# Kernel tuning notes

Measured on AMD Instinct MI355X. Metric: run time of the kernel, lower is better.

Reference implementation:

```python
import jax, jax.numpy as jnp
import numpy as np

NUM_HEADS = 4
GROUPS = 8          # min(8, ch) with ch=256
EPS = 1e-5          # torch GroupNorm default eps


def setup_inputs() -> dict:
    key = jax.random.key(0)
    ks = jax.random.split(key, 3)
    b, c, h, w = 8, 256, 32, 32
    x = jax.random.normal(ks[0], (b, c, h, w), jnp.float32)
    gn_gamma = jnp.ones((c,), jnp.float32)
    gn_beta = jnp.zeros((c,), jnp.float32)
    qkv_w = jax.random.normal(ks[1], (3 * c, c), jnp.float32) * (c ** -0.5)
    qkv_b = jnp.zeros((3 * c,), jnp.float32)
    proj_w = jax.random.normal(ks[2], (c, c), jnp.float32) * (c ** -0.5)
    proj_b = jnp.zeros((c,), jnp.float32)
    return {"x": x, "gn_gamma": gn_gamma, "gn_beta": gn_beta,
            "qkv_w": qkv_w, "qkv_b": qkv_b, "proj_w": proj_w, "proj_b": proj_b}


def _group_norm(x, gamma, beta):
    b, c, h, w = x.shape
    xg = x.reshape(b, GROUPS, c // GROUPS, h, w)
    mean = xg.mean(axis=(2, 3, 4), keepdims=True)
    var = xg.var(axis=(2, 3, 4), keepdims=True)
    xn = ((xg - mean) * jax.lax.rsqrt(var + EPS)).reshape(b, c, h, w)
    return xn * gamma[None, :, None, None] + beta[None, :, None, None]


def reference(x, gn_gamma, gn_beta, qkv_w, qkv_b, proj_w, proj_b):
    b, c, h, w = x.shape
    dh = c // NUM_HEADS
    xn = _group_norm(x, gn_gamma, gn_beta)
    # 1x1 conv == channel matmul
    qkv = jnp.einsum('oc,bchw->bohw', qkv_w, xn) + qkv_b[None, :, None, None]
    qkv = qkv.reshape(b, 3, NUM_HEADS, dh, h * w)
    q, k, v = qkv[:, 0], qkv[:, 1], qkv[:, 2]   # each (b, n, dh, hw)
    scale = dh ** -0.5
    # full (hw x hw) attention matrix, matching the original explicit einsum
    attn = jax.nn.softmax(jnp.einsum('bncd,bnce->bnde', q, k) * scale, axis=-1)
    out = jnp.einsum('bnde,bnce->bncd', attn, v).reshape(b, c, h, w)
    out = jnp.einsum('oc,bchw->bohw', proj_w, out) + proj_b[None, :, None, None]
    return x + out
```

## Files before the change

kernel.cpp:

```cpp
#include <hip/hip_runtime.h>
#include <stdint.h>

typedef __attribute__((ext_vector_type(8))) short short8;
typedef __attribute__((ext_vector_type(4))) float f32x4;

#define BB 8
#define CC 256
#define PP 1024
#define NH 4
#define DH 64

#define QSCALE 0.18033688f

__device__ __forceinline__ unsigned short f2bf(float f) {
  union { float f; unsigned u; } v; v.f = f;
  unsigned r = v.u + 0x7FFFu + ((v.u >> 16) & 1u);
  return (unsigned short)(r >> 16);
}

__device__ __forceinline__ f32x4 mfma16(short8 a, short8 b, f32x4 c) {
  return __builtin_amdgcn_mfma_f32_16x16x32_bf16(a, b, c, 0, 0, 0);
}

__global__ __launch_bounds__(256) void prep(
    const float* __restrict__ x, float2* __restrict__ part,
    const float* __restrict__ qkvw, const float* __restrict__ projw,
    unsigned short* __restrict__ wall) {
  int blk = blockIdx.x;
  int tid = threadIdx.x;
  if (blk < 512) {
    int sl = blk & 7, g = (blk >> 3) & 7, b = blk >> 6;
    const float4* xb =
        (const float4*)(x + (size_t)(b * CC + g * 32) * PP) + sl * 1024;
    float s = 0.f, q = 0.f;
    for (int i = tid; i < 1024; i += 256) {
      float4 v = xb[i];
      s += v.x + v.y + v.z + v.w;
      q += v.x * v.x + v.y * v.y + v.z * v.z + v.w * v.w;
    }
    for (int off = 32; off > 0; off >>= 1) {
      s += __shfl_down(s, off);
      q += __shfl_down(q, off);
    }
    __shared__ float rs[4], rq[4];
    int w = tid >> 6;
    if ((tid & 63) == 0) { rs[w] = s; rq[w] = q; }
    __syncthreads();
    if (tid == 0)
      part[blk] = make_float2(rs[0] + rs[1] + rs[2] + rs[3],
                              rq[0] + rq[1] + rq[2] + rq[3]);
  } else {
    int i4 = (blk - 512) * 256 + tid;
    float4 v = (i4 < 49152) ? ((const float4*)qkvw)[i4]
                            : ((const float4*)projw)[i4 - 49152];
    ushort4 o;
    o.x = f2bf(v.x); o.y = f2bf(v.y); o.z = f2bf(v.z); o.w = f2bf(v.w);
    ((ushort4*)wall)[i4] = o;
  }
}

__global__ __launch_bounds__(256) void nqkv(
    const float* __restrict__ x, const float2* __restrict__ part,
    const float* __restrict__ gamma, const float* __restrict__ beta,
    const unsigned short* __restrict__ wbf, const float* __restrict__ qkvb,
    unsigned short* __restrict__ qb, unsigned short* __restrict__ kb,
    unsigned short* __restrict__ vT) {
  int p0 = blockIdx.x * 128, o0 = blockIdx.y * 128, b = blockIdx.z;
  int tid = threadIdx.x;
  int w = tid >> 6, lane = tid & 63, lq = lane >> 4, ln = lane & 15;
  int wy = w >> 1, wx = w & 1;
  __shared__ unsigned short A_l[128][40];
  __shared__ unsigned short B_l[128][40];
  __shared__ float scs[256], shs[256];
  __shared__ float g_m[8], g_r[8];
  if (tid < 8) {
    float S = 0.f, Q = 0.f;
    for (int i = 0; i < 8; ++i) {
      float2 pp = part[b * 64 + tid * 8 + i];
      S += pp.x; Q += pp.y;
    }
    float mean = S * (1.f / 32768.f);
    float var = Q * (1.f / 32768.f) - mean * mean;
    g_m[tid] = mean;
    g_r[tid] = rsqrtf(var + 1e-5f);
  }
  __syncthreads();
  {
    int c = tid;
    float sc = g_r[c >> 5] * gamma[c];
    scs[c] = sc;
    shs[c] = beta[c] - g_m[c >> 5] * sc;
  }
  __syncthreads();
  f32x4 acc[4][4];
  for (int i = 0; i < 4; ++i)
    for (int j = 0; j < 4; ++j) acc[i][j] = (f32x4){0.f, 0.f, 0.f, 0.f};
  int cc = tid >> 3, ps = tid & 7;
  for (int kc = 0; kc < 256; kc += 32) {
    {
      float sc = scs[kc + cc], sh = shs[kc + cc];
      const float* xr = x + ((size_t)(b * CC + kc + cc)) * PP + p0;
#pragma unroll
      for (int i = 0; i < 4; ++i) {
        int p = ps * 4 + 32 * i;
        float4 v = *(const float4*)(xr + p);
        A_l[p + 0][cc] = f2bf(v.x * sc + sh);
        A_l[p + 1][cc] = f2bf(v.y * sc + sh);
        A_l[p + 2][cc] = f2bf(v.z * sc + sh);
        A_l[p + 3][cc] = f2bf(v.w * sc + sh);
      }
    }
    for (int it = 0; it < 2; ++it) {
      int l = tid + 256 * it;
      int row = l >> 2, seg = l & 3;
      *(short8*)&B_l[row][seg * 8] =
          *(const short8*)(wbf + (size_t)(o0 + row) * CC + kc + seg * 8);
    }
    __syncthreads();
    short8 af[4], bfr[4];
    for (int i = 0; i < 4; ++i)
      af[i] = *(const short8*)&A_l[wy * 64 + i * 16 + ln][lq * 8];
    for (int j = 0; j < 4; ++j)
      bfr[j] = *(const short8*)&B_l[wx * 64 + j * 16 + ln][lq * 8];
    for (int i = 0; i < 4; ++i)
      for (int j = 0; j < 4; ++j) acc[i][j] = mfma16(af[i], bfr[j], acc[i][j]);
    __syncthreads();
  }
  for (int i = 0; i < 4; ++i) {
    for (int j = 0; j < 4; ++j) {
      int o = o0 + wx * 64 + j * 16 + ln;
      int s = o >> 8, h = (o >> 6) & 3, ch = o & 63;
      float bias = qkvb[o];
      float mul = (s == 0) ? QSCALE : 1.0f;
      size_t bh = (size_t)b * NH + h;
      int pbase = p0 + wy * 64 + i * 16 + lq * 4;
      if (s == 2) {
        union { unsigned short u[4]; unsigned long long ll; } pk;
#pragma unroll
        for (int r = 0; r < 4; ++r) pk.u[r] = f2bf(acc[i][j][r] + bias);
        *(unsigned long long*)(vT + (bh * DH + ch) * PP + pbase) = pk.ll;
      } else {
        unsigned short* dst = (s == 0) ? qb : kb;
#pragma unroll
        for (int r = 0; r < 4; ++r)
          dst[(bh * PP + pbase + r) * DH + ch] =
              f2bf((acc[i][j][r] + bias) * mul);
      }
    }
  }
}

__global__ __launch_bounds__(256) void attn(
    const unsigned short* __restrict__ qb, const unsigned short* __restrict__ kb,
    const unsigned short* __restrict__ vT, unsigned short* __restrict__ attnT) {
  int d0 = blockIdx.x * 64, h = blockIdx.y, b = blockIdx.z;
  int tid = threadIdx.x;
  int w = tid >> 6, lane = tid & 63, lq = lane >> 4, ln = lane & 15;
  size_t bh = (size_t)b * NH + h;
  const unsigned short* qbase = qb + bh * PP * DH;
  const unsigned short* kbase = kb + bh * PP * DH;
  const unsigned short* vbase = vT + bh * DH * PP;
  __shared__ unsigned short K_l[128][72];
  __shared__ unsigned short V_l[64][136];
  __shared__ unsigned short P_l[64][140];
  unsigned short (*O_l)[72] = (unsigned short (*)[72]) & P_l[0][0];

  int ke = tid >> 1, kseg = tid & 1;
  int vch = tid >> 2, vseg = tid & 3;

  short8 qf[2];
  {
    int d = d0 + w * 16 + ln;
    qf[0] = *(const short8*)(qbase + (size_t)d * DH + lq * 8);
    qf[1] = *(const short8*)(qbase + (size_t)d * DH + 32 + lq * 8);
  }
  float l_sum = 0.f;
  f32x4 o_acc[4];
  for (int i = 0; i < 4; ++i) o_acc[i] = (f32x4){0.f, 0.f, 0.f, 0.f};

  short8 kr[4], vr[4];
#pragma unroll
  for (int i = 0; i < 4; ++i)
    kr[i] = *(const short8*)(kbase + (size_t)ke * DH + kseg * 32 + i * 8);
#pragma unroll
  for (int i = 0; i < 4; ++i)
    vr[i] = *(const short8*)(vbase + (size_t)vch * PP + vseg * 32 + i * 8);

  for (int e0 = 0; e0 < PP; e0 += 128) {
#pragma unroll
    for (int i = 0; i < 4; ++i)
      *(short8*)&K_l[ke][kseg * 32 + i * 8] = kr[i];
#pragma unroll
    for (int i = 0; i < 4; ++i)
      *(short8*)&V_l[vch][vseg * 32 + i * 8] = vr[i];
    if (e0 + 128 < PP) {
      int en = e0 + 128;
#pragma unroll
      for (int i = 0; i < 4; ++i)
        kr[i] = *(const short8*)(kbase + (size_t)(en + ke) * DH + kseg * 32 + i * 8);
#pragma unroll
      for (int i = 0; i < 4; ++i)
        vr[i] = *(const short8*)(vbase + (size_t)vch * PP + en + vseg * 32 + i * 8);
    }
    __syncthreads();
    f32x4 sc[8];
#pragma unroll
    for (int ns = 0; ns < 8; ++ns) {
      f32x4 a = (f32x4){0.f, 0.f, 0.f, 0.f};
      a = mfma16(*(const short8*)&K_l[ns * 16 + ln][lq * 8], qf[0], a);
      a = mfma16(*(const short8*)&K_l[ns * 16 + ln][32 + lq * 8], qf[1], a);
      sc[ns] = a;
    }
#pragma unroll
    for (int ns = 0; ns < 8; ++ns) {
      float p0 = __builtin_amdgcn_exp2f(fminf(sc[ns][0], 86.f));
      float p1 = __builtin_amdgcn_exp2f(fminf(sc[ns][1], 86.f));
      float p2 = __builtin_amdgcn_exp2f(fminf(sc[ns][2], 86.f));
      float p3 = __builtin_amdgcn_exp2f(fminf(sc[ns][3], 86.f));
      l_sum += (p0 + p1) + (p2 + p3);
      union { unsigned short u[4]; unsigned long long ll; } pk;
      pk.u[0] = f2bf(p0); pk.u[1] = f2bf(p1);
      pk.u[2] = f2bf(p2); pk.u[3] = f2bf(p3);
      *(unsigned long long*)&P_l[w * 16 + ln][ns * 16 + lq * 4] = pk.ll;
    }
#pragma unroll
    for (int t = 0; t < 4; ++t) {
      short8 pb = *(const short8*)&P_l[w * 16 + ln][t * 32 + lq * 8];
#pragma unroll
      for (int cs = 0; cs < 4; ++cs)
        o_acc[cs] = mfma16(
            *(const short8*)&V_l[cs * 16 + ln][t * 32 + lq * 8], pb, o_acc[cs]);
    }
    __syncthreads();
  }
  float rsum = l_sum;
  rsum += __shfl_xor(rsum, 16);
  rsum += __shfl_xor(rsum, 32);
  float inv = 1.f / rsum;
#pragma unroll
  for (int cs = 0; cs < 4; ++cs) {
    union { unsigned short u[4]; unsigned long long ll; } pk;
#pragma unroll
    for (int r = 0; r < 4; ++r) pk.u[r] = f2bf(o_acc[cs][r] * inv);
    *(unsigned long long*)&O_l[w * 16 + ln][cs * 16 + lq * 4] = pk.ll;
  }
  __syncthreads();
  for (int it = 0; it < 2; ++it) {
    int l = tid + 256 * it;
    int dd = l >> 3, seg = l & 7;
    *(short8*)(attnT + ((size_t)b * PP + d0 + dd) * CC + h * DH + seg * 8) =
        *(const short8*)&O_l[dd][seg * 8];
  }
}

__global__ __launch_bounds__(256) void proj_gemm(
    const unsigned short* __restrict__ attnT, const unsigned short* __restrict__ pwbf,
    const float* __restrict__ projb, const float* __restrict__ x,
    float* __restrict__ out) {
  int p0 = blockIdx.x * 128, o0 = blockIdx.y * 64, b = blockIdx.z;
  int tid = threadIdx.x;
  int w = tid >> 6, lane = tid & 63, lq = lane >> 4, ln = lane & 15;
  __shared__ unsigned short A_l[64][40];
  __shared__ unsigned short B_l[128][40];
  f32x4 acc[4][2];
  for (int i = 0; i < 4; ++i)
    for (int j = 0; j < 2; ++j) acc[i][j] = (f32x4){0.f, 0.f, 0.f, 0.f};
  for (int kc = 0; kc < 256; kc += 32) {
    {
      int row = tid >> 2, seg = tid & 3;
      *(short8*)&A_l[row][seg * 8] =
          *(const short8*)(pwbf + (size_t)(o0 + row) * CC + kc + seg * 8);
    }
    for (int it = 0; it < 2; ++it) {
      int l = tid + 256 * it;
      int row = l >> 2, seg = l & 3;
      *(short8*)&B_l[row][seg * 8] =
          *(const short8*)(attnT + ((size_t)b * PP + p0 + row) * CC + kc + seg * 8);
    }
    __syncthreads();
    short8 af[4], bfr[2];
    for (int i = 0; i < 4; ++i)
      af[i] = *(const short8*)&A_l[i * 16 + ln][lq * 8];
    for (int j = 0; j < 2; ++j)
      bfr[j] = *(const short8*)&B_l[w * 32 + j * 16 + ln][lq * 8];
    for (int i = 0; i < 4; ++i)
      for (int j = 0; j < 2; ++j) acc[i][j] = mfma16(af[i], bfr[j], acc[i][j]);
    __syncthreads();
  }
  for (int i = 0; i < 4; ++i) {
    for (int j = 0; j < 2; ++j) {
      int p = p0 + w * 32 + j * 16 + ln;
      for (int r = 0; r < 4; ++r) {
        int o = o0 + i * 16 + lq * 4 + r;
        size_t idx = ((size_t)b * CC + o) * PP + p;
        out[idx] = x[idx] + projb[o] + acc[i][j][r];
      }
    }
  }
}

extern "C" void kernel_launch(void* const* d_in, const int* in_sizes, int n_in,
                              void* d_out, int out_size, void* d_ws, size_t ws_size,
                              hipStream_t stream) {
  const float* x = (const float*)d_in[0];
  const float* gamma = (const float*)d_in[1];
  const float* beta = (const float*)d_in[2];
  const float* qkvw = (const float*)d_in[3];
  const float* qkvb = (const float*)d_in[4];
  const float* projw = (const float*)d_in[5];
  const float* projb = (const float*)d_in[6];
  float* out = (float*)d_out;
  char* ws = (char*)d_ws;

  float2* part = (float2*)(ws + 0);
  unsigned short* wall = (unsigned short*)(ws + 4210688);
  unsigned short* pwbf = wall + 768 * 256;
  unsigned short* qb = (unsigned short*)(ws + 4734976);
  unsigned short* kb = (unsigned short*)(ws + 8929280);
  unsigned short* vT = (unsigned short*)(ws + 13123584);
  unsigned short* attnT = (unsigned short*)(ws + 17317888);

  prep<<<768, 256, 0, stream>>>(x, part, qkvw, projw, wall);
  nqkv<<<dim3(8, 6, 8), 256, 0, stream>>>(x, part, gamma, beta, wall, qkvb,
                                          qb, kb, vT);
  attn<<<dim3(16, 4, 8), 256, 0, stream>>>(qb, kb, vT, attnT);
  proj_gemm<<<dim3(8, 4, 8), 256, 0, stream>>>(attnT, pwbf, projb, x, out);
}
```

Baseline: 119.7 us.

## Rewrite attention kernel with 32x32 MFMA, register-resident P, and split-key reduction

Moves the attention inner loop from 16x16x32 to 32x32x16 bf16 MFMA and splits the 4 waves into 2 query halves by 2 key halves. The softmax probabilities are packed straight into MFMA operand registers, so the P staging through shared memory is gone. K and V tiles use XOR-swizzled shared-memory layouts to avoid bank conflicts. Partial outputs and row sums are combined across the key-split waves through shared memory at the end. Shared memory shrinks to 32KB and launch bounds ask for 2 blocks per CU, at the cost of larger accumulators and an extra final reduction.

```diff
diff --git a/kernel.cpp b/kernel.cpp
--- a/kernel.cpp
+++ b/kernel.cpp
@@ -3,6 +3,8 @@
 
 typedef __attribute__((ext_vector_type(8))) short short8;
 typedef __attribute__((ext_vector_type(4))) float f32x4;
+typedef __attribute__((ext_vector_type(16))) float f32x16;
+typedef unsigned long long u64;
 
 #define BB 8
 #define CC 256
@@ -20,6 +22,9 @@
 
 __device__ __forceinline__ f32x4 mfma16(short8 a, short8 b, f32x4 c) {
   return __builtin_amdgcn_mfma_f32_16x16x32_bf16(a, b, c, 0, 0, 0);
+}
+__device__ __forceinline__ f32x16 mfma32(short8 a, short8 b, f32x16 c) {
+  return __builtin_amdgcn_mfma_f32_32x32x16_bf16(a, b, c, 0, 0, 0);
 }
 
 __global__ __launch_bounds__(256) void prep(
@@ -135,10 +140,10 @@
       size_t bh = (size_t)b * NH + h;
       int pbase = p0 + wy * 64 + i * 16 + lq * 4;
       if (s == 2) {
-        union { unsigned short u[4]; unsigned long long ll; } pk;
+        union { unsigned short u[4]; u64 ll; } pk;
 #pragma unroll
         for (int r = 0; r < 4; ++r) pk.u[r] = f2bf(acc[i][j][r] + bias);
-        *(unsigned long long*)(vT + (bh * DH + ch) * PP + pbase) = pk.ll;
+        *(u64*)(vT + (bh * DH + ch) * PP + pbase) = pk.ll;
       } else {
         unsigned short* dst = (s == 0) ? qb : kb;
 #pragma unroll
@@ -150,33 +155,43 @@
   }
 }
 
-__global__ __launch_bounds__(256) void attn(
+__global__ __launch_bounds__(256, 2) void attn(
     const unsigned short* __restrict__ qb, const unsigned short* __restrict__ kb,
     const unsigned short* __restrict__ vT, unsigned short* __restrict__ attnT) {
   int d0 = blockIdx.x * 64, h = blockIdx.y, b = blockIdx.z;
   int tid = threadIdx.x;
-  int w = tid >> 6, lane = tid & 63, lq = lane >> 4, ln = lane & 15;
+  int w = tid >> 6, lane = tid & 63;
+  int n = lane & 31, hi = lane >> 5;
+  int wd = w & 1, we = w >> 1;
   size_t bh = (size_t)b * NH + h;
   const unsigned short* qbase = qb + bh * PP * DH;
   const unsigned short* kbase = kb + bh * PP * DH;
   const unsigned short* vbase = vT + bh * DH * PP;
-  __shared__ unsigned short K_l[128][72];
-  __shared__ unsigned short V_l[64][136];
-  __shared__ unsigned short P_l[64][140];
-  unsigned short (*O_l)[72] = (unsigned short (*)[72]) & P_l[0][0];
+
+  __shared__ __align__(16) char smem[32768];
+  unsigned short* K_ls = (unsigned short*)smem;
+  unsigned short* V_ls = (unsigned short*)(smem + 16384);
+  float* Ored = (float*)smem;
+  float* lsred = (float*)(smem + 17408);
+  unsigned short* O_l = (unsigned short*)(smem + 17664);
+
+#define KIDX(e, cb) ((e) * 64 + (((cb) ^ ((e) & 7)) << 3))
+#define VIDX(ch, cb, off) ((ch) * 128 + (((cb) ^ ((ch) & 7)) << 3) + (off))
 
   int ke = tid >> 1, kseg = tid & 1;
   int vch = tid >> 2, vseg = tid & 3;
 
-  short8 qf[2];
+  short8 qf[4];
   {
-    int d = d0 + w * 16 + ln;
-    qf[0] = *(const short8*)(qbase + (size_t)d * DH + lq * 8);
-    qf[1] = *(const short8*)(qbase + (size_t)d * DH + 32 + lq * 8);
+    int dq = d0 + wd * 32 + n;
+#pragma unroll
+    for (int kc = 0; kc < 4; ++kc)
+      qf[kc] = *(const short8*)(qbase + (size_t)dq * DH + kc * 16 + hi * 8);
   }
   float l_sum = 0.f;
-  f32x4 o_acc[4];
-  for (int i = 0; i < 4; ++i) o_acc[i] = (f32x4){0.f, 0.f, 0.f, 0.f};
+  f32x16 o_acc[2];
+#pragma unroll
+  for (int i = 0; i < 16; ++i) { o_acc[0][i] = 0.f; o_acc[1][i] = 0.f; }
 
   short8 kr[4], vr[4];
 #pragma unroll
@@ -189,10 +204,16 @@
   for (int e0 = 0; e0 < PP; e0 += 128) {
 #pragma unroll
     for (int i = 0; i < 4; ++i)
-      *(short8*)&K_l[ke][kseg * 32 + i * 8] = kr[i];
-#pragma unroll
-    for (int i = 0; i < 4; ++i)
-      *(short8*)&V_l[vch][vseg * 32 + i * 8] = vr[i];
+      *(short8*)&K_ls[KIDX(ke, kseg * 4 + i)] = kr[i];
+#pragma unroll
+    for (int i = 0; i < 4; ++i) {
+      int acb = vseg * 4 + i;
+      int blkA = acb >> 1;
+      int h8 = acb & 1;
+      union { short8 v; u64 q[2]; } uv; uv.v = vr[i];
+      *(u64*)&V_ls[VIDX(vch, blkA * 2 + 0, h8 * 4)] = uv.q[0];
+      *(u64*)&V_ls[VIDX(vch, blkA * 2 + 1, h8 * 4)] = uv.q[1];
+    }
     if (e0 + 128 < PP) {
       int en = e0 + 128;
 #pragma unroll
@@ -203,54 +224,88 @@
         vr[i] = *(const short8*)(vbase + (size_t)vch * PP + en + vseg * 32 + i * 8);
     }
     __syncthreads();
-    f32x4 sc[8];
-#pragma unroll
-    for (int ns = 0; ns < 8; ++ns) {
-      f32x4 a = (f32x4){0.f, 0.f, 0.f, 0.f};
-      a = mfma16(*(const short8*)&K_l[ns * 16 + ln][lq * 8], qf[0], a);
-      a = mfma16(*(const short8*)&K_l[ns * 16 + ln][32 + lq * 8], qf[1], a);
-      sc[ns] = a;
-    }
-#pragma unroll
-    for (int ns = 0; ns < 8; ++ns) {
-      float p0 = __builtin_amdgcn_exp2f(fminf(sc[ns][0], 86.f));
-      float p1 = __builtin_amdgcn_exp2f(fminf(sc[ns][1], 86.f));
-      float p2 = __builtin_amdgcn_exp2f(fminf(sc[ns][2], 86.f));
-      float p3 = __builtin_amdgcn_exp2f(fminf(sc[ns][3], 86.f));
-      l_sum += (p0 + p1) + (p2 + p3);
-      union { unsigned short u[4]; unsigned long long ll; } pk;
-      pk.u[0] = f2bf(p0); pk.u[1] = f2bf(p1);
-      pk.u[2] = f2bf(p2); pk.u[3] = f2bf(p3);
-      *(unsigned long long*)&P_l[w * 16 + ln][ns * 16 + lq * 4] = pk.ll;
-    }
-#pragma unroll
-    for (int t = 0; t < 4; ++t) {
-      short8 pb = *(const short8*)&P_l[w * 16 + ln][t * 32 + lq * 8];
-#pragma unroll
-      for (int cs = 0; cs < 4; ++cs)
-        o_acc[cs] = mfma16(
-            *(const short8*)&V_l[cs * 16 + ln][t * 32 + lq * 8], pb, o_acc[cs]);
-    }
-    __syncthreads();
-  }
-  float rsum = l_sum;
-  rsum += __shfl_xor(rsum, 16);
-  rsum += __shfl_xor(rsum, 32);
-  float inv = 1.f / rsum;
-#pragma unroll
-  for (int cs = 0; cs < 4; ++cs) {
-    union { unsigned short u[4]; unsigned long long ll; } pk;
-#pragma unroll
-    for (int r = 0; r < 4; ++r) pk.u[r] = f2bf(o_acc[cs][r] * inv);
-    *(unsigned long long*)&O_l[w * 16 + ln][cs * 16 + lq * 4] = pk.ll;
+    u64 pk[2][4];
+#pragma unroll
+    for (int t = 0; t < 2; ++t) {
+      f32x16 s;
+#pragma unroll
+      for (int i = 0; i < 16; ++i) s[i] = 0.f;
+      int erow = we * 64 + t * 32 + n;
+#pragma unroll
+      for (int kc = 0; kc < 4; ++kc) {
+        short8 af = *(const short8*)&K_ls[KIDX(erow, kc * 2 + hi)];
+        s = mfma32(af, qf[kc], s);
+      }
+#pragma unroll
+      for (int g = 0; g < 4; ++g) {
+        float p0 = __builtin_amdgcn_exp2f(fminf(s[4 * g + 0], 86.f));
+        float p1 = __builtin_amdgcn_exp2f(fminf(s[4 * g + 1], 86.f));
+        float p2 = __builtin_amdgcn_exp2f(fminf(s[4 * g + 2], 86.f));
+        float p3 = __builtin_amdgcn_exp2f(fminf(s[4 * g + 3], 86.f));
+        l_sum += (p0 + p1) + (p2 + p3);
+        union { unsigned short u[4]; u64 ll; } pkk;
+        pkk.u[0] = f2bf(p0); pkk.u[1] = f2bf(p1);
+        pkk.u[2] = f2bf(p2); pkk.u[3] = f2bf(p3);
+        pk[t][g] = pkk.ll;
+      }
+    }
+#pragma unroll
+    for (int t = 0; t < 2; ++t) {
+#pragma unroll
+      for (int c = 0; c < 2; ++c) {
+        union { u64 q[2]; short8 v; } pf;
+        pf.q[0] = pk[t][2 * c];
+        pf.q[1] = pk[t][2 * c + 1];
+        int cb = we * 8 + t * 4 + c * 2 + hi;
+#pragma unroll
+        for (int mt = 0; mt < 2; ++mt) {
+          int ch = mt * 32 + n;
+          short8 af = *(const short8*)&V_ls[VIDX(ch, cb, 0)];
+          o_acc[mt] = mfma32(af, pf.v, o_acc[mt]);
+        }
+      }
+    }
+    __syncthreads();
+  }
+  l_sum += __shfl_xor(l_sum, 32);
+  if (we == 1) {
+    if (hi == 0) lsred[wd * 32 + n] = l_sum;
+#pragma unroll
+    for (int mt = 0; mt < 2; ++mt)
+#pragma unroll
+      for (int r = 0; r < 16; ++r) {
+        int chl = (r & 3) + 8 * (r >> 2) + 4 * hi;
+        Ored[(wd * 64 + mt * 32 + chl) * 34 + n] = o_acc[mt][r];
+      }
+  }
+  __syncthreads();
+  if (we == 0) {
+    float inv = 1.f / (l_sum + lsred[wd * 32 + n]);
+#pragma unroll
+    for (int mt = 0; mt < 2; ++mt) {
+#pragma unroll
+      for (int g = 0; g < 4; ++g) {
+        union { unsigned short u[4]; u64 ll; } pkk;
+#pragma unroll
+        for (int q = 0; q < 4; ++q) {
+          int r = g * 4 + q;
+          int chl = q + 8 * g + 4 * hi;
+          float v = (o_acc[mt][r] + Ored[(wd * 64 + mt * 32 + chl) * 34 + n]) * inv;
+          pkk.u[q] = f2bf(v);
+        }
+        *(u64*)&O_l[(wd * 32 + n) * 72 + mt * 32 + g * 8 + 4 * hi] = pkk.ll;
+      }
+    }
   }
   __syncthreads();
   for (int it = 0; it < 2; ++it) {
-    int l = tid + 256 * it;
-    int dd = l >> 3, seg = l & 7;
+    int l2 = tid + 256 * it;
+    int dd = l2 >> 3, seg = l2 & 7;
     *(short8*)(attnT + ((size_t)b * PP + d0 + dd) * CC + h * DH + seg * 8) =
-        *(const short8*)&O_l[dd][seg * 8];
-  }
+        *(const short8*)&O_l[dd * 72 + seg * 8];
+  }
+#undef KIDX
+#undef VIDX
 }
 
 __global__ __launch_bounds__(256) void proj_gemm(
```

Result: no change. 118.3 us (-1.1%).
